# Kernel optimization log

Hardware: AMD Instinct MI355X
Metric: run time of the kernel (lower is better)

Reference implementation:

```python
import jax, jax.numpy as jnp
import numpy as np

DIM = 512
HEADS = 8
HEAD_DIM = DIM // HEADS
SCALE = DIM ** (-0.5)  # source uses full dim, not head_dim
LAMBDA_COND = 1.0


def setup_inputs() -> dict:
    key = jax.random.key(0)
    ks = jax.random.split(key, 16)
    b, n, m_a, m_s = 4, 2048, 2048, 256
    s = 0.02
    inp = {
        "x": jax.random.normal(ks[0], (b, n, DIM), jnp.float32),
        "audio_context": jax.random.normal(ks[1], (b, m_a, DIM), jnp.float32),
        "singer_context": jax.random.normal(ks[2], (b, m_s, DIM), jnp.float32),
        "Wq": jax.random.normal(ks[3], (DIM, DIM), jnp.float32) * s,
        "bq": jnp.zeros((DIM,), jnp.float32),
        "Wka": jax.random.normal(ks[4], (DIM, DIM), jnp.float32) * s,
        "bka": jnp.zeros((DIM,), jnp.float32),
        "Wva": jax.random.normal(ks[5], (DIM, DIM), jnp.float32) * s,
        "bva": jnp.zeros((DIM,), jnp.float32),
        "Wks": jax.random.normal(ks[6], (DIM, DIM), jnp.float32) * s,
        "bks": jnp.zeros((DIM,), jnp.float32),
        "Wvs": jax.random.normal(ks[7], (DIM, DIM), jnp.float32) * s,
        "bvs": jnp.zeros((DIM,), jnp.float32),
        "Wp": jax.random.normal(ks[8], (DIM, DIM), jnp.float32) * s,
        "bp": jnp.zeros((DIM,), jnp.float32),
    }
    return inp


def _heads(t):
    b, n, c = t.shape
    return t.reshape(b, n, HEADS, HEAD_DIM).transpose(0, 2, 1, 3)  # (b,h,n,d)


def _attend(q, ctx, Wk, bk, Wv, bv):
    k = _heads(ctx @ Wk.T + bk)
    v = _heads(ctx @ Wv.T + bv)
    attn = jax.nn.softmax(jnp.einsum("bhnd,bhmd->bhnm", q, k) * SCALE, axis=-1)
    o = jnp.einsum("bhnm,bhmd->bhnd", attn, v)
    b, h, n, d = o.shape
    return o.transpose(0, 2, 1, 3).reshape(b, n, h * d)


def reference(x, audio_context, singer_context, Wq, bq, Wka, bka, Wva, bva,
              Wks, bks, Wvs, bvs, Wp, bp):
    q = _heads(x @ Wq.T + bq)
    x_audio = _attend(q, audio_context, Wka, bka, Wva, bva)
    x_singer = _attend(q, singer_context, Wks, bks, Wvs, bvs)
    out = x_audio + LAMBDA_COND * x_singer
    return out @ Wp.T + bp
```

## Files before the change

kernel.cpp:

```cpp
#include <hip/hip_runtime.h>

#define DIM 512
#define NQ 2048
#define MA 2048
#define MS 256
#define QSCALE 0.06375864651f

typedef __attribute__((ext_vector_type(8))) short bf16x8;
typedef __attribute__((ext_vector_type(4))) float f32x4;
typedef __attribute__((ext_vector_type(16))) float f32x16;

__device__ __forceinline__ ushort f2b(float f) {
    uint u = __float_as_uint(f);
    u = (u + 0x7fffu + ((u >> 16) & 1u)) >> 16;
    return (ushort)u;
}

__device__ __forceinline__ uint pk2bf(float a, float b) {
#if __has_builtin(__builtin_amdgcn_cvt_pk_bf16_f32)
    typedef __attribute__((ext_vector_type(2))) __bf16 bf2;
    bf2 r = __builtin_amdgcn_cvt_pk_bf16_f32(a, b);
    uint u;
    __builtin_memcpy(&u, &r, 4);
    return u;
#else
    return ((__float_as_uint(a) + 0x8000u) >> 16) |
           ((__float_as_uint(b) + 0x8000u) & 0xffff0000u);
#endif
}

__device__ __forceinline__ float fexp2(float x) {
#if __has_builtin(__builtin_amdgcn_exp2f)
    return __builtin_amdgcn_exp2f(x);
#else
    return exp2f(x);
#endif
}

__device__ __forceinline__ void gload16(const ushort* g, ushort* l) {
    __builtin_amdgcn_global_load_lds(
        (const __attribute__((address_space(1))) void*)g,
        (__attribute__((address_space(3))) void*)l, 16, 0, 0);
}

__global__ __launch_bounds__(256) void cast_all(const float* __restrict__ w0,
                                                const float* __restrict__ w1,
                                                const float* __restrict__ w2,
                                                const float* __restrict__ w3,
                                                const float* __restrict__ w4,
                                                const float* __restrict__ w5,
                                                const float* __restrict__ x,
                                                const float* __restrict__ ac,
                                                const float* __restrict__ scx,
                                                ushort* __restrict__ dst) {
    int i = blockIdx.x * 256 + threadIdx.x;
    const float* s;
    int o;
    if (i < 393216) {
        int w = i >> 16;
        s = w < 3 ? (w == 0 ? w0 : (w == 1 ? w1 : w2))
                  : (w == 3 ? w3 : (w == 4 ? w4 : w5));
        o = i & 65535;
    } else if (i < 1441792) { s = x;   o = i - 393216; }
    else if (i < 2490368)   { s = ac;  o = i - 1441792; }
    else                    { s = scx; o = i - 2490368; }
    float4 v = ((const float4*)s)[o];
    ushort4 u;
    u.x = f2b(v.x); u.y = f2b(v.y); u.z = f2b(v.z); u.w = f2b(v.w);
    ((ushort4*)dst)[i] = u;
}

struct GD {
    const ushort* A; const ushort* B; const float* bias; void* out;
    long sB, sO;
    int N, bx, by, blk0, biasrow, scaleq, outf32, permc;
};

__global__ __launch_bounds__(256) void gemm_fused(GD d0, GD d1, GD d2, GD d3, GD d4) {
    __shared__ ushort At[128 * 32];
    __shared__ ushort Bt[128 * 32];
    GD d = d0;
    int bid = blockIdx.x;
    if (bid >= d1.blk0) d = d1;
    if (bid >= d2.blk0) d = d2;
    if (bid >= d3.blk0) d = d3;
    if (bid >= d4.blk0) d = d4;
    int local = bid - d.blk0;
    int x = local % d.bx;
    int rem = local / d.bx;
    int y = rem % d.by;
    int z = rem / d.by;

    int t = threadIdx.x;
    int wv = t >> 6, ln = t & 63, l = ln & 15, g = ln >> 4;
    int wrow = wv & 1, wcol = wv >> 1;
    int row0 = x * 128, col0 = y * 128;
    int srow = t >> 2;
    int slot = (t & 3) * 8;
    int sko = ((t ^ srow) & 3) * 8;
    int kc8 = ((g ^ (l & 3)) & 3) * 8;
    int l4 = (l >> 2) & 3;
    int lp = d.permc ? (l4 == 1 ? l + 4 : (l4 == 2 ? l - 4 : l)) : l;
    const ushort* Ab = d.A;
    const ushort* Bb = d.B + (size_t)z * d.sB;
    int N = d.N;

    f32x4 acc[4][4];
#pragma unroll
    for (int i = 0; i < 4; i++)
#pragma unroll
        for (int j = 0; j < 4; j++) acc[i][j] = (f32x4){0, 0, 0, 0};

    for (int k0 = 0; k0 < 512; k0 += 32) {
        __syncthreads();
#pragma unroll
        for (int c = 0; c < 2; c++) {
            gload16(Ab + (size_t)(row0 + srow + 64 * c) * 512 + k0 + sko,
                    At + (srow + 64 * c) * 32 + slot);
            gload16(Bb + (size_t)(col0 + srow + 64 * c) * 512 + k0 + sko,
                    Bt + (srow + 64 * c) * 32 + slot);
        }
        __syncthreads();
        bf16x8 ar[4], br[4];
#pragma unroll
        for (int i = 0; i < 4; i++)
            ar[i] = *(const bf16x8*)(At + (wrow * 64 + i * 16 + l) * 32 + kc8);
#pragma unroll
        for (int j = 0; j < 4; j++)
            br[j] = *(const bf16x8*)(Bt + (wcol * 64 + j * 16 + l) * 32 + kc8);
#pragma unroll
        for (int i = 0; i < 4; i++)
#pragma unroll
            for (int j = 0; j < 4; j++)
                acc[i][j] = __builtin_amdgcn_mfma_f32_16x16x32_bf16(ar[i], br[j], acc[i][j], 0, 0, 0);
    }
#pragma unroll
    for (int i = 0; i < 4; i++) {
#pragma unroll
        for (int j = 0; j < 4; j++) {
            int row = row0 + wrow * 64 + i * 16 + g * 4;
            int col = col0 + wcol * 64 + j * 16 + lp;
#pragma unroll
            for (int r = 0; r < 4; r++) {
                float bv = d.biasrow ? d.bias[row + r] : d.bias[col];
                float o = acc[i][j][r] + bv;
                if (d.scaleq) o *= QSCALE;
                if (d.outf32)
                    ((float*)d.out + (size_t)z * d.sO)[(size_t)(row + r) * N + col] = o;
                else
                    ((ushort*)d.out + (size_t)z * d.sO)[(size_t)(row + r) * N + col] = f2b(o);
            }
        }
    }
}

__device__ __forceinline__ void attn_64q(const ushort* __restrict__ kgb,
                                         const ushort* __restrict__ vgb,
                                         int M, int nt, const bf16x8 (&aq)[2][4],
                                         ushort* __restrict__ Kl,
                                         ushort* __restrict__ Vl,
                                         f32x16 (&o)[4], float (&li)[2],
                                         int l5, int hi, int w, int ln) {
    int r8 = ln >> 3;
    int cc = 8 * ((ln & 7) ^ r8);
    const ushort* ks0 = kgb + (size_t)(w * 16 + r8) * DIM + cc;
    const ushort* vs0 = vgb + (size_t)(w * 16 + r8) * M + cc;
    int rx = (l5 & 7) * 8;
    int hb = hi * 8;
    gload16(ks0, Kl + w * 1024);
    gload16(ks0 + (size_t)8 * DIM, Kl + w * 1024 + 512);
    gload16(vs0, Vl + w * 1024);
    gload16(vs0 + (size_t)8 * M, Vl + w * 1024 + 512);
    for (int i = 0; i < nt; i++) {
        __syncthreads();
        if (i + 1 < nt) {
            const ushort* ks = ks0 + (size_t)(i + 1) * 64 * DIM;
            const ushort* vs = vs0 + (size_t)(i + 1) * 64;
            ushort* Kb = Kl + ((i + 1) & 1) * 4096;
            ushort* Vb = Vl + ((i + 1) & 1) * 4096;
            gload16(ks, Kb + w * 1024);
            gload16(ks + (size_t)8 * DIM, Kb + w * 1024 + 512);
            gload16(vs, Vb + w * 1024);
            gload16(vs + (size_t)8 * M, Vb + w * 1024 + 512);
        }
        const ushort* Kc = Kl + (i & 1) * 4096;
        const ushort* Vc = Vl + (i & 1) * 4096;
        uint2 pq[2][2][4];
#pragma unroll
        for (int c = 0; c < 2; c++) {
            bf16x8 kf[4];
#pragma unroll
            for (int kd = 0; kd < 4; kd++)
                kf[kd] = *(const bf16x8*)(Kc + (32 * c + l5) * 64 + ((kd * 16 + hb) ^ rx));
#pragma unroll
            for (int qh = 0; qh < 2; qh++) {
                f32x16 s;
#pragma unroll
                for (int ii = 0; ii < 16; ii++) s[ii] = 0.f;
                __builtin_amdgcn_s_setprio(1);
#pragma unroll
                for (int kd = 0; kd < 4; kd++)
                    s = __builtin_amdgcn_mfma_f32_32x32x16_bf16(kf[kd], aq[qh][kd], s, 0, 0, 0);
                __builtin_amdgcn_s_setprio(0);
#pragma unroll
                for (int m = 0; m < 4; m++) {
                    float p0 = fexp2(s[4 * m + 0]);
                    float p1 = fexp2(s[4 * m + 1]);
                    float p2 = fexp2(s[4 * m + 2]);
                    float p3 = fexp2(s[4 * m + 3]);
                    li[qh] += (p0 + p1) + (p2 + p3);
                    pq[qh][c][m].x = pk2bf(p0, p1);
                    pq[qh][c][m].y = pk2bf(p2, p3);
                }
            }
        }
#pragma unroll
        for (int kc = 0; kc < 4; kc++) {
            int c = kc >> 1, m0 = 2 * (kc & 1);
            bf16x8 vf0 = *(const bf16x8*)(Vc + l5 * 64 + ((kc * 16 + hb) ^ rx));
            bf16x8 vf1 = *(const bf16x8*)(Vc + (32 + l5) * 64 + ((kc * 16 + hb) ^ rx));
            __builtin_amdgcn_s_setprio(1);
#pragma unroll
            for (int qh = 0; qh < 2; qh++) {
                union { bf16x8 v; uint u[4]; } wv;
                wv.u[0] = pq[qh][c][m0].x;     wv.u[1] = pq[qh][c][m0].y;
                wv.u[2] = pq[qh][c][m0 + 1].x; wv.u[3] = pq[qh][c][m0 + 1].y;
                o[qh * 2 + 0] = __builtin_amdgcn_mfma_f32_32x32x16_bf16(wv.v, vf0, o[qh * 2 + 0], 0, 0, 0);
                o[qh * 2 + 1] = __builtin_amdgcn_mfma_f32_32x32x16_bf16(wv.v, vf1, o[qh * 2 + 1], 0, 0, 0);
            }
            __builtin_amdgcn_s_setprio(0);
        }
    }
}

__global__ __launch_bounds__(512) void attn_kernel(const ushort* __restrict__ q,
                                                   const ushort* __restrict__ Ka,
                                                   const ushort* __restrict__ VTa,
                                                   const ushort* __restrict__ Ks,
                                                   const ushort* __restrict__ VTs,
                                                   ushort* __restrict__ y) {
    __shared__ ushort smem[67584];
    int t = threadIdx.x;
    int grp = t >> 8;
    int tg = t & 255;
    int w = (t >> 6) & 3;
    int ln = t & 63, l5 = ln & 31, hi = ln >> 5;
    ushort* Kl = smem + grp * 16384;
    ushort* Vl = Kl + 8192;
    float* Bx = (float*)(smem + 32768);
    float* Ax = (float*)smem;
    int h = blockIdx.y, bi = blockIdx.z;
    int q0w = blockIdx.x * 256 + w * 64;

    bf16x8 aq[2][4];
#pragma unroll
    for (int qh = 0; qh < 2; qh++) {
        const ushort* qp = q + (size_t)(bi * NQ + q0w + qh * 32 + l5) * DIM + h * 64 + hi * 8;
#pragma unroll
        for (int kd = 0; kd < 4; kd++) aq[qh][kd] = *(const bf16x8*)(qp + kd * 16);
    }

    f32x16 o[4];
#pragma unroll
    for (int k = 0; k < 4; k++)
#pragma unroll
        for (int i = 0; i < 16; i++) o[k][i] = 0.f;
    float li[2] = {0.f, 0.f};

    attn_64q(Ka + (size_t)bi * MA * DIM + (size_t)(grp * 1024) * DIM + h * 64,
             VTa + (size_t)bi * DIM * MA + (size_t)(h * 64) * MA + grp * 1024,
             MA, 16, aq, Kl, Vl, o, li, l5, hi, w, ln);
    li[0] += __shfl_xor(li[0], 32);
    li[1] += __shfl_xor(li[1], 32);
    __syncthreads();
    float* slot = Bx + tg * 68;
    if (grp) {
#pragma unroll
        for (int k = 0; k < 4; k++)
#pragma unroll
            for (int r = 0; r < 8; r++)
                *(float2*)(slot + k * 16 + 2 * r) = (float2){o[k][2 * r], o[k][2 * r + 1]};
        slot[64] = li[0];
        slot[65] = li[1];
    }
    __syncthreads();
    if (!grp) {
#pragma unroll
        for (int k = 0; k < 4; k++)
#pragma unroll
            for (int r = 0; r < 16; r++) o[k][r] += slot[k * 16 + r];
        li[0] += slot[64];
        li[1] += slot[65];
#pragma unroll
        for (int qh = 0; qh < 2; qh++) {
            float inv[16];
#pragma unroll
            for (int rg = 0; rg < 16; rg++)
                inv[rg] = 1.f / __shfl(li[qh], (rg & 3) + 8 * (rg >> 2) + 4 * hi);
#pragma unroll
            for (int dn = 0; dn < 2; dn++)
#pragma unroll
                for (int rg = 0; rg < 16; rg++) o[qh * 2 + dn][rg] *= inv[rg];
        }
#pragma unroll
        for (int k = 0; k < 4; k++)
#pragma unroll
            for (int r = 0; r < 8; r++)
                *(float2*)(slot + k * 16 + 2 * r) = (float2){o[k][2 * r], o[k][2 * r + 1]};
    }

#pragma unroll
    for (int k = 0; k < 4; k++)
#pragma unroll
        for (int i = 0; i < 16; i++) o[k][i] = 0.f;
    li[0] = li[1] = 0.f;
    attn_64q(Ks + (size_t)bi * MS * DIM + (size_t)(grp * 128) * DIM + h * 64,
             VTs + (size_t)bi * DIM * MS + (size_t)(h * 64) * MS + grp * 128,
             MS, 2, aq, Kl, Vl, o, li, l5, hi, w, ln);
    li[0] += __shfl_xor(li[0], 32);
    li[1] += __shfl_xor(li[1], 32);
    __syncthreads();
    float* As = Ax + tg * 64;
    if (grp) {
#pragma unroll
        for (int k = 0; k < 4; k++)
#pragma unroll
            for (int r = 0; r < 8; r++)
                *(float2*)(As + k * 16 + 2 * r) = (float2){o[k][2 * r], o[k][2 * r + 1]};
        slot[66] = li[0];
        slot[67] = li[1];
    }
    __syncthreads();
    if (!grp) {
#pragma unroll
        for (int k = 0; k < 4; k++)
#pragma unroll
            for (int r = 0; r < 16; r++) o[k][r] += As[k * 16 + r];
        li[0] += slot[66];
        li[1] += slot[67];
#pragma unroll
        for (int qh = 0; qh < 2; qh++) {
            float inv[16];
#pragma unroll
            for (int rg = 0; rg < 16; rg++)
                inv[rg] = 1.f / __shfl(li[qh], (rg & 3) + 8 * (rg >> 2) + 4 * hi);
#pragma unroll
            for (int dn = 0; dn < 2; dn++)
#pragma unroll
                for (int rg = 0; rg < 16; rg++) {
                    int qr = (rg & 3) + 8 * (rg >> 2) + 4 * hi;
                    float ov = slot[(qh * 2 + dn) * 16 + rg] + o[qh * 2 + dn][rg] * inv[rg];
                    y[(size_t)(bi * NQ + q0w + qh * 32 + qr) * DIM + h * 64 + 32 * dn + l5] = f2b(ov);
                }
        }
    }
}

extern "C" void kernel_launch(void* const* d_in, const int* in_sizes, int n_in,
                              void* d_out, int out_size, void* d_ws, size_t ws_size,
                              hipStream_t stream) {
    const float* x   = (const float*)d_in[0];
    const float* ac  = (const float*)d_in[1];
    const float* scx = (const float*)d_in[2];
    const float* Wq  = (const float*)d_in[3];
    const float* bq  = (const float*)d_in[4];
    const float* Wka = (const float*)d_in[5];
    const float* bka = (const float*)d_in[6];
    const float* Wva = (const float*)d_in[7];
    const float* bva = (const float*)d_in[8];
    const float* Wks = (const float*)d_in[9];
    const float* bks = (const float*)d_in[10];
    const float* Wvs = (const float*)d_in[11];
    const float* bvs = (const float*)d_in[12];
    const float* Wp  = (const float*)d_in[13];
    const float* bp  = (const float*)d_in[14];

    ushort* wb   = (ushort*)d_ws;
    ushort* wqb  = wb;
    ushort* wkab = wb + 262144;
    ushort* wvab = wb + 2 * 262144;
    ushort* wksb = wb + 3 * 262144;
    ushort* wvsb = wb + 4 * 262144;
    ushort* wpb  = wb + 5 * 262144;
    ushort* xb   = wb + 6 * 262144;
    ushort* acb  = xb + 4194304;
    ushort* scxb = acb + 4194304;
    ushort* qb   = scxb + 524288;
    ushort* kab  = qb + 4194304;
    ushort* vta  = kab + 4194304;
    ushort* ksb  = vta + 4194304;
    ushort* vts  = ksb + 524288;
    ushort* yb   = xb;

    cast_all<<<10240, 256, 0, stream>>>(Wq, Wka, Wva, Wks, Wvs, Wp, x, ac, scx, wb);

    GD gq   = {xb,   wqb,  bq,  qb,  0, 0,               512,  64, 4,  0,   0, 1, 0, 0};
    GD gka  = {acb,  wkab, bka, kab, 0, 0,               512,  64, 4,  256, 0, 0, 0, 0};
    GD gvta = {wvab, acb,  bva, vta, 2048L * 512, 512L * 2048, 2048, 4, 16, 512, 1, 0, 0, 1};
    GD gks  = {scxb, wksb, bks, ksb, 0, 0,               512,  8,  4,  768, 0, 0, 0, 0};
    GD gvts = {wvsb, scxb, bvs, vts, 256L * 512, 512L * 256,   256,  4,  2,  800, 1, 0, 0, 1};
    gemm_fused<<<832, 256, 0, stream>>>(gq, gka, gvta, gks, gvts);

    attn_kernel<<<dim3(8, 8, 4), 512, 0, stream>>>(qb, kab, vta, ksb, vts, yb);

    GD gpr = {yb, wpb, bp, d_out, 0, 0, 512, 64, 4, 0, 0, 0, 1, 0};
    GD gnv = {nullptr, nullptr, nullptr, nullptr, 0, 0, 0, 1, 1, 1 << 30, 0, 0, 0, 0};
    gemm_fused<<<256, 256, 0, stream>>>(gpr, gnv, gnv, gnv, gnv);
}
```

Baseline: 226.7 us.

## Double-buffer LDS tiles in fused GEMM to overlap loads with MFMA

Splits the A and B shared-memory tiles into two buffers and prefetches the next K-slice into the idle buffer while MFMAs consume the current one. This removes one of the two barriers per K iteration. Loop-invariant row pointers are hoisted out of the loop. It doubles LDS use per block, which may lower occupancy, and correctness depends on the global-to-LDS loads having completed before the next barrier.

```diff
diff --git a/kernel.cpp b/kernel.cpp
--- a/kernel.cpp
+++ b/kernel.cpp
@@ -77,8 +77,8 @@
 };
 
 __global__ __launch_bounds__(256) void gemm_fused(GD d0, GD d1, GD d2, GD d3, GD d4) {
-    __shared__ ushort At[128 * 32];
-    __shared__ ushort Bt[128 * 32];
+    __shared__ ushort At[2][128 * 32];
+    __shared__ ushort Bt[2][128 * 32];
     GD d = d0;
     int bid = blockIdx.x;
     if (bid >= d1.blk0) d = d1;
@@ -105,29 +105,41 @@
     const ushort* Bb = d.B + (size_t)z * d.sB;
     int N = d.N;
 
+    const ushort* Ar0 = Ab + (size_t)(row0 + srow) * 512 + sko;
+    const ushort* Ar1 = Ab + (size_t)(row0 + srow + 64) * 512 + sko;
+    const ushort* Br0 = Bb + (size_t)(col0 + srow) * 512 + sko;
+    const ushort* Br1 = Bb + (size_t)(col0 + srow + 64) * 512 + sko;
+    int so0 = srow * 32 + slot;
+    int so1 = (srow + 64) * 32 + slot;
+
     f32x4 acc[4][4];
 #pragma unroll
     for (int i = 0; i < 4; i++)
 #pragma unroll
         for (int j = 0; j < 4; j++) acc[i][j] = (f32x4){0, 0, 0, 0};
 
+    gload16(Ar0, At[0] + so0);
+    gload16(Ar1, At[0] + so1);
+    gload16(Br0, Bt[0] + so0);
+    gload16(Br1, Bt[0] + so1);
+
+#pragma unroll 2
     for (int k0 = 0; k0 < 512; k0 += 32) {
+        int cur = (k0 >> 5) & 1;
         __syncthreads();
-#pragma unroll
-        for (int c = 0; c < 2; c++) {
-            gload16(Ab + (size_t)(row0 + srow + 64 * c) * 512 + k0 + sko,
-                    At + (srow + 64 * c) * 32 + slot);
-            gload16(Bb + (size_t)(col0 + srow + 64 * c) * 512 + k0 + sko,
-                    Bt + (srow + 64 * c) * 32 + slot);
-        }
-        __syncthreads();
+        if (k0 + 32 < 512) {
+            gload16(Ar0 + k0 + 32, At[cur ^ 1] + so0);
+            gload16(Ar1 + k0 + 32, At[cur ^ 1] + so1);
+            gload16(Br0 + k0 + 32, Bt[cur ^ 1] + so0);
+            gload16(Br1 + k0 + 32, Bt[cur ^ 1] + so1);
+        }
         bf16x8 ar[4], br[4];
 #pragma unroll
         for (int i = 0; i < 4; i++)
-            ar[i] = *(const bf16x8*)(At + (wrow * 64 + i * 16 + l) * 32 + kc8);
+            ar[i] = *(const bf16x8*)(At[cur] + (wrow * 64 + i * 16 + l) * 32 + kc8);
 #pragma unroll
         for (int j = 0; j < 4; j++)
-            br[j] = *(const bf16x8*)(Bt + (wcol * 64 + j * 16 + l) * 32 + kc8);
+            br[j] = *(const bf16x8*)(Bt[cur] + (wcol * 64 + j * 16 + l) * 32 + kc8);
 #pragma unroll
         for (int i = 0; i < 4; i++)
 #pragma unroll
```

Result: no change. 225.2 us (median of 2 runs) (-0.7%).
